# Kernel tuning notes

Measured on AMD Instinct MI355X. Metric: run time of the kernel, lower is better.

The kernel has to match this reference:

```python
import jax, jax.numpy as jnp
import numpy as np

N_NODES = 1000
N_EDGES = 8000
BATCH = 64
IN_DIM = 64
HID = 128
N_CLASSES = 2


def setup_inputs() -> dict:
    key = jax.random.key(0)
    ks = jax.random.split(key, 8)
    x = jax.random.normal(ks[0], (BATCH * N_NODES, IN_DIM), jnp.float32)
    # per-graph random edges, offset so each graph's nodes are disjoint
    ei = jax.random.randint(ks[1], (2, BATCH * N_EDGES), 0, N_NODES)
    offs = jnp.repeat(jnp.arange(BATCH) * N_NODES, N_EDGES)
    edge_index = (ei + offs[None, :]).astype(jnp.int32)
    batch = jnp.repeat(jnp.arange(BATCH), N_NODES).astype(jnp.int32)
    # learnable params (init is ones in source; use uniform [0,1.3] to exercise
    # both the <0.2 zeroing branch and the clamp-at-1 branch)
    edge_weights = jax.random.uniform(ks[2], (N_EDGES,), jnp.float32, 0.0, 1.3)
    node_importance = jax.random.uniform(ks[3], (N_NODES,), jnp.float32, 0.0, 1.3)
    s1 = 1.0 / np.sqrt(IN_DIM)
    W1 = jax.random.uniform(ks[4], (IN_DIM, HID), jnp.float32, -s1, s1)
    b1 = jnp.zeros((HID,), jnp.float32)
    sn = 1.0 / np.sqrt(HID * N_NODES)
    Wn = jax.random.uniform(ks[5], (HID * N_NODES, 32), jnp.float32, -sn, sn)
    bn = jnp.zeros((32,), jnp.float32)
    sc = 1.0 / np.sqrt(32)
    Wc = jax.random.uniform(ks[6], (32, N_CLASSES), jnp.float32, -sc, sc)
    bc = jnp.zeros((N_CLASSES,), jnp.float32)
    return dict(x=x, edge_index=edge_index, batch=batch,
                edge_weights=edge_weights, node_importance=node_importance,
                W1=W1, b1=b1, Wn=Wn, bn=bn, Wc=Wc, bc=bc)


def _gcn(x, src, dst, ew, W, b, n):
    """PyG GCNConv: add self-loops (weight 1), symmetric normalization, linear."""
    loop = jnp.arange(n, dtype=src.dtype)
    src = jnp.concatenate([src, loop])
    dst = jnp.concatenate([dst, loop])
    ew = jnp.concatenate([ew, jnp.ones((n,), ew.dtype)])
    deg = jax.ops.segment_sum(ew, dst, num_segments=n)
    dinv = jnp.where(deg > 0, jax.lax.rsqrt(jnp.maximum(deg, 1e-12)), 0.0)
    norm = dinv[src] * ew * dinv[dst]          # [E+n]
    h = x @ W                                  # [n, HID]
    out = jax.ops.segment_sum(h[src] * norm[:, None], dst, num_segments=n)
    return out + b


def reference(x, edge_index, batch, edge_weights, node_importance,
              W1, b1, Wn, bn, Wc, bc):
    # edge sparsification: zero below 0.2, clamp above at 1
    ew = jnp.where(edge_weights < 0.2, 0.0, jnp.minimum(edge_weights, 1.0))
    ni_clamped = jnp.clip(node_importance, 0.0, 1.0)
    B = edge_index.shape[1] // N_EDGES
    n_total = x.shape[0]
    exp_ew = jnp.tile(ew, B)
    # source uses the RAW (unclamped) node_importance here - replicated
    exp_ni = jnp.tile(node_importance, B)[:, None]
    h = x * exp_ni
    h = _gcn(h, edge_index[0], edge_index[1], exp_ew, W1, b1, n_total)
    h = jax.nn.relu(h)
    # each graph has exactly N_NODES nodes and batch is sorted, so the
    # per-graph mask+pad loop is exactly a reshape
    g = h.reshape(B, N_NODES * h.shape[1])     # [B, N*HID]
    g = g @ Wn + bn                            # [B, 32]
    out = g @ Wc + bc                          # [B, N_CLASSES]
    return (out, ew, ni_clamped)
```

## Files before the change

### kernel.cpp

```cpp
#include <hip/hip_runtime.h>

#define N_NODES_C 1000
#define N_EDGES_C 8000
#define BATCH_C   64
#define IN_DIM_C  64
#define HID_C     128
#define NT (BATCH_C * N_NODES_C)
#define ET (BATCH_C * N_EDGES_C)

#define WS_DEG    0
#define WS_EWS    64000
#define WS_ROWP   72000
#define WS_PEDGE  137536
#define WS_PART   1161536
#define WS_H2     1685824

__global__ __launch_bounds__(256) void prep(const float* __restrict__ ew_in,
                                            const float* __restrict__ ni,
                                            float* __restrict__ ws,
                                            float* __restrict__ out) {
    int i = blockIdx.x * 256 + threadIdx.x;
    if (i < N_EDGES_C) {
        float w = ew_in[i];
        float s = (w < 0.2f) ? 0.0f : fminf(w, 1.0f);
        ws[WS_EWS + i] = s;
        out[128 + i] = s;
    }
    if (i < N_NODES_C) {
        float v = ni[i];
        out[128 + N_EDGES_C + i] = fminf(fmaxf(v, 0.0f), 1.0f);
    }
}

__global__ __launch_bounds__(256) void deg_csr(const int* __restrict__ ei,
                                               float* __restrict__ ws) {
    __shared__ float dacc[N_NODES_C];
    __shared__ int   cnt[N_NODES_C];
    __shared__ int   rs[N_NODES_C + 8];
    __shared__ int   wtot[4];
    int g = blockIdx.x, tid = threadIdx.x;
    int lane = tid & 63, wid = tid >> 6;
    int ebase = g * N_EDGES_C, gbase = g * N_NODES_C;
    const float* ews = ws + WS_EWS;

    for (int i = tid; i < N_NODES_C; i += 256) { dacc[i] = 1.0f; cnt[i] = 0; }
    __syncthreads();

    for (int le = tid; le < N_EDGES_C; le += 256) {
        int dl = ei[ET + ebase + le] - gbase;
        atomicAdd(&dacc[dl], ews[le]);
        atomicAdd(&cnt[dl], 1);
    }
    __syncthreads();

    for (int i = tid; i < N_NODES_C; i += 256) {
        float d = rsqrtf(dacc[i]);
        dacc[i] = d;
        ws[WS_DEG + gbase + i] = d;
    }

    int s0 = 0, s1 = 0, s2 = 0, s3 = 0, tsum = 0;
    if (tid < 250) {
        s0 = cnt[4 * tid]; s1 = cnt[4 * tid + 1];
        s2 = cnt[4 * tid + 2]; s3 = cnt[4 * tid + 3];
        tsum = s0 + s1 + s2 + s3;
    }
    int v = tsum;
    #pragma unroll
    for (int off = 1; off < 64; off <<= 1) {
        int n = __shfl_up(v, off, 64);
        if (lane >= off) v += n;
    }
    if (lane == 63) wtot[wid] = v;
    __syncthreads();
    int base = 0;
    for (int w = 0; w < wid; ++w) base += wtot[w];
    int excl = base + v - tsum;
    if (tid < 250) {
        rs[4 * tid]     = excl;
        rs[4 * tid + 1] = excl + s0;
        rs[4 * tid + 2] = excl + s0 + s1;
        rs[4 * tid + 3] = excl + s0 + s1 + s2;
    }
    if (tid == 255) rs[N_NODES_C] = N_EDGES_C;
    __syncthreads();

    int* rowp = (int*)(ws + WS_ROWP);
    for (int i = tid; i <= N_NODES_C; i += 256) rowp[g * 1024 + i] = rs[i];
    for (int i = tid; i < N_NODES_C; i += 256) cnt[i] = rs[i];
    __syncthreads();

    int2* pedge = (int2*)(ws + WS_PEDGE);
    for (int le = tid; le < N_EDGES_C; le += 256) {
        int s  = ei[ebase + le];
        int dl = ei[ET + ebase + le] - gbase;
        float nm = dacc[s - gbase] * ews[le] * dacc[dl];
        int pos = atomicAdd(&cnt[dl], 1);
        pedge[ebase + pos] = make_int2(s, __float_as_int(nm));
    }
}

__global__ __launch_bounds__(256) void gemm_h2(const float* __restrict__ x,
                                               const float* __restrict__ ni,
                                               const float* __restrict__ W1,
                                               float* __restrict__ h2) {
    __shared__ float xs[128][65];
    __shared__ float wsm[64 * 128];
    int tid = threadIdx.x;
    int base = blockIdx.x * 128;

    #pragma unroll
    for (int i = 0; i < 8; ++i) {
        int idx = i * 1024 + tid * 4;
        int r = idx >> 6, d = idx & 63;
        float4 v = *(const float4*)&x[(base + r) * 64 + d];
        float s = ni[(base + r) % N_NODES_C];
        xs[r][d + 0] = v.x * s;
        xs[r][d + 1] = v.y * s;
        xs[r][d + 2] = v.z * s;
        xs[r][d + 3] = v.w * s;
    }
    #pragma unroll
    for (int i = 0; i < 8; ++i) {
        int idx = i * 1024 + tid * 4;
        *(float4*)&wsm[idx] = *(const float4*)&W1[idx];
    }
    __syncthreads();

    int tx = tid & 15, ty = tid >> 4;
    int r0 = ty * 8, c0 = tx * 8;
    float acc[8][8];
    #pragma unroll
    for (int i = 0; i < 8; ++i)
        #pragma unroll
        for (int j = 0; j < 8; ++j) acc[i][j] = 0.0f;

    for (int d = 0; d < 64; ++d) {
        float a[8];
        #pragma unroll
        for (int i = 0; i < 8; ++i) a[i] = xs[r0 + i][d];
        float4 b0 = *(float4*)&wsm[d * 128 + c0];
        float4 b1 = *(float4*)&wsm[d * 128 + c0 + 4];
        float b[8] = {b0.x, b0.y, b0.z, b0.w, b1.x, b1.y, b1.z, b1.w};
        #pragma unroll
        for (int i = 0; i < 8; ++i)
            #pragma unroll
            for (int j = 0; j < 8; ++j)
                acc[i][j] = fmaf(a[i], b[j], acc[i][j]);
    }

    #pragma unroll
    for (int i = 0; i < 8; ++i) {
        float* dst = &h2[(base + r0 + i) * HID_C + c0];
        float4 o0 = {acc[i][0], acc[i][1], acc[i][2], acc[i][3]};
        float4 o1 = {acc[i][4], acc[i][5], acc[i][6], acc[i][7]};
        *(float4*)dst = o0;
        *(float4*)(dst + 4) = o1;
    }
}

__global__ __launch_bounds__(256) void spmm(const float* __restrict__ ws_ro,
                                            float* __restrict__ h2,
                                            const float* __restrict__ b1) {
    __shared__ float res[N_NODES_C * 16];
    int bid = blockIdx.x;
    int g  = bid & 63;
    int c0 = (bid >> 6) * 16;
    int tid = threadIdx.x;
    int fq = tid & 3, dslot = tid >> 2;

    const int*  rowp  = (const int*)(ws_ro + WS_ROWP) + g * 1024;
    const int2* pedge = (const int2*)(ws_ro + WS_PEDGE) + g * N_EDGES_C;
    const float* dinv = ws_ro + WS_DEG;
    int gbase = g * N_NODES_C;

    for (int iter = 0; iter < 16; ++iter) {
        int d = iter * 64 + dslot;
        if (d < N_NODES_C) {
            int e0 = rowp[d], e1 = rowp[d + 1];
            float4 a = make_float4(0.f, 0.f, 0.f, 0.f);
            for (int e = e0; e < e1; ++e) {
                int2 ed = pedge[e];
                float nm = __int_as_float(ed.y);
                float4 hv = *(const float4*)&h2[ed.x * HID_C + c0 + fq * 4];
                a.x = fmaf(hv.x, nm, a.x);
                a.y = fmaf(hv.y, nm, a.y);
                a.z = fmaf(hv.z, nm, a.z);
                a.w = fmaf(hv.w, nm, a.w);
            }
            *(float4*)&res[d * 16 + fq * 4] = a;
        }
    }
    __syncthreads();

    for (int idx = tid; idx < N_NODES_C * 16; idx += 256) {
        int v = idx >> 4, f = idx & 15;
        int node = gbase + v;
        float dv = dinv[node];
        float val = res[idx] + h2[node * HID_C + c0 + f] * (dv * dv) + b1[c0 + f];
        h2[node * HID_C + c0 + f] = fmaxf(val, 0.0f);
    }
}

__global__ __launch_bounds__(256) void reduce_g(const float* __restrict__ rh,
                                                const float* __restrict__ Wn,
                                                float* __restrict__ part) {
    int tid = threadIdx.x;
    int j = tid & 31, bg = tid >> 5;
    int k0 = blockIdx.x * 500;
    float acc[8] = {0, 0, 0, 0, 0, 0, 0, 0};
    for (int kk = 0; kk < 500; kk += 4) {
        int k = k0 + kk;
        float w0 = Wn[(k + 0) * 32 + j];
        float w1 = Wn[(k + 1) * 32 + j];
        float w2 = Wn[(k + 2) * 32 + j];
        float w3 = Wn[(k + 3) * 32 + j];
        #pragma unroll
        for (int u = 0; u < 8; ++u) {
            float4 r = *(const float4*)&rh[(bg * 8 + u) * 128000 + k];
            acc[u] = fmaf(r.x, w0, acc[u]);
            acc[u] = fmaf(r.y, w1, acc[u]);
            acc[u] = fmaf(r.z, w2, acc[u]);
            acc[u] = fmaf(r.w, w3, acc[u]);
        }
    }
    #pragma unroll
    for (int u = 0; u < 8; ++u)
        part[blockIdx.x * 2048 + (bg * 8 + u) * 32 + j] = acc[u];
}

__global__ __launch_bounds__(256) void final_out(const float* __restrict__ ws_ro,
                                                 const float* __restrict__ bn,
                                                 const float* __restrict__ Wc,
                                                 const float* __restrict__ bc,
                                                 float* __restrict__ out) {
    int gid = blockIdx.x * 256 + threadIdx.x;
    int g = gid >> 5, j = gid & 31;
    const float* part = ws_ro + WS_PART;
    float s = 0.0f;
    for (int c = 0; c < 256; ++c)
        s += part[c * 2048 + gid];
    float gv = s + bn[j];
    float o0 = gv * Wc[j * 2 + 0];
    float o1 = gv * Wc[j * 2 + 1];
    #pragma unroll
    for (int off = 16; off >= 1; off >>= 1) {
        o0 += __shfl_xor(o0, off);
        o1 += __shfl_xor(o1, off);
    }
    if (j == 0) {
        out[g * 2 + 0] = o0 + bc[0];
        out[g * 2 + 1] = o1 + bc[1];
    }
}

extern "C" void kernel_launch(void* const* d_in, const int* in_sizes, int n_in,
                              void* d_out, int out_size, void* d_ws, size_t ws_size,
                              hipStream_t stream) {
    const float* x  = (const float*)d_in[0];
    const int*   ei = (const int*)d_in[1];
    const float* ew = (const float*)d_in[3];
    const float* ni = (const float*)d_in[4];
    const float* W1 = (const float*)d_in[5];
    const float* b1 = (const float*)d_in[6];
    const float* Wn = (const float*)d_in[7];
    const float* bn = (const float*)d_in[8];
    const float* Wc = (const float*)d_in[9];
    const float* bc = (const float*)d_in[10];
    float* out = (float*)d_out;
    float* ws  = (float*)d_ws;

    prep<<<32, 256, 0, stream>>>(ew, ni, ws, out);
    gemm_h2<<<NT / 128, 256, 0, stream>>>(x, ni, W1, ws + WS_H2);
    deg_csr<<<BATCH_C, 256, 0, stream>>>(ei, ws);
    spmm<<<BATCH_C * 8, 256, 0, stream>>>(ws, ws + WS_H2, b1);
    reduce_g<<<256, 256, 0, stream>>>(ws + WS_H2, Wn, ws + WS_PART);
    final_out<<<8, 256, 0, stream>>>(ws, bn, Wc, bc, out);
}
```

Before: 293.3 us.

## Split CSR build into grid-wide kernels and add out-of-place SpMM path

Replaces the per-graph single-block degree/CSR kernel (64 blocks) with three grid-wide kernels: a global-atomic degree/count pass, a per-graph scan, and a global-atomic scatter. When the workspace is large enough, a new out-of-place SpMM runs with one thread per (node, 16-feature chunk) and writes to a separate buffer, so it needs no shared staging and no block-wide sync. Otherwise an in-place fallback runs with 1024-thread blocks. The aim is better GPU occupancy for the graph preprocessing and aggregation, at the cost of extra launches and contended global atomics.

Measured after the change: 258.9 us. 1.13x faster.

```diff
diff --git a/kernel.cpp b/kernel.cpp
--- a/kernel.cpp
+++ b/kernel.cpp
@@ -10,16 +10,23 @@
 
 #define WS_DEG    0
 #define WS_EWS    64000
-#define WS_ROWP   72000
-#define WS_PEDGE  137536
-#define WS_PART   1161536
-#define WS_H2     1685824
+#define WS_CNT    72000
+#define WS_CUR    136000
+#define WS_ROWP   200000
+#define WS_PEDGE  265536
+#define WS_PART   1289536
+#define WS_H2     1813824
+#define WS_RH     10005824
 
 __global__ __launch_bounds__(256) void prep(const float* __restrict__ ew_in,
                                             const float* __restrict__ ni,
                                             float* __restrict__ ws,
                                             float* __restrict__ out) {
     int i = blockIdx.x * 256 + threadIdx.x;
+    if (i < NT) {
+        ws[WS_DEG + i] = 1.0f;
+        ((int*)(ws + WS_CNT))[i] = 0;
+    }
     if (i < N_EDGES_C) {
         float w = ew_in[i];
         float s = (w < 0.2f) ? 0.0f : fminf(w, 1.0f);
@@ -32,32 +39,25 @@
     }
 }
 
-__global__ __launch_bounds__(256) void deg_csr(const int* __restrict__ ei,
+__global__ __launch_bounds__(256) void deg_cnt(const int* __restrict__ ei,
                                                float* __restrict__ ws) {
-    __shared__ float dacc[N_NODES_C];
-    __shared__ int   cnt[N_NODES_C];
-    __shared__ int   rs[N_NODES_C + 8];
-    __shared__ int   wtot[4];
+    int e = blockIdx.x * 256 + threadIdx.x;
+    int d = ei[ET + e];
+    int le = e % N_EDGES_C;
+    atomicAdd(&ws[WS_DEG + d], ws[WS_EWS + le]);
+    atomicAdd(&((int*)(ws + WS_CNT))[d], 1);
+}
+
+__global__ __launch_bounds__(256) void csr_scan(float* __restrict__ ws) {
+    __shared__ int rs[N_NODES_C + 8];
+    __shared__ int wtot[4];
     int g = blockIdx.x, tid = threadIdx.x;
     int lane = tid & 63, wid = tid >> 6;
-    int ebase = g * N_EDGES_C, gbase = g * N_NODES_C;
-    const float* ews = ws + WS_EWS;
-
-    for (int i = tid; i < N_NODES_C; i += 256) { dacc[i] = 1.0f; cnt[i] = 0; }
-    __syncthreads();
-
-    for (int le = tid; le < N_EDGES_C; le += 256) {
-        int dl = ei[ET + ebase + le] - gbase;
-        atomicAdd(&dacc[dl], ews[le]);
-        atomicAdd(&cnt[dl], 1);
-    }
-    __syncthreads();
-
-    for (int i = tid; i < N_NODES_C; i += 256) {
-        float d = rsqrtf(dacc[i]);
-        dacc[i] = d;
-        ws[WS_DEG + gbase + i] = d;
-    }
+    int gbase = g * N_NODES_C;
+    const int* cnt = (const int*)(ws + WS_CNT) + gbase;
+
+    for (int i = tid; i < N_NODES_C; i += 256)
+        ws[WS_DEG + gbase + i] = rsqrtf(ws[WS_DEG + gbase + i]);
 
     int s0 = 0, s1 = 0, s2 = 0, s3 = 0, tsum = 0;
     if (tid < 250) {
@@ -85,19 +85,24 @@
     if (tid == 255) rs[N_NODES_C] = N_EDGES_C;
     __syncthreads();
 
-    int* rowp = (int*)(ws + WS_ROWP);
-    for (int i = tid; i <= N_NODES_C; i += 256) rowp[g * 1024 + i] = rs[i];
-    for (int i = tid; i < N_NODES_C; i += 256) cnt[i] = rs[i];
-    __syncthreads();
-
-    int2* pedge = (int2*)(ws + WS_PEDGE);
-    for (int le = tid; le < N_EDGES_C; le += 256) {
-        int s  = ei[ebase + le];
-        int dl = ei[ET + ebase + le] - gbase;
-        float nm = dacc[s - gbase] * ews[le] * dacc[dl];
-        int pos = atomicAdd(&cnt[dl], 1);
-        pedge[ebase + pos] = make_int2(s, __float_as_int(nm));
-    }
+    int* rowp = (int*)(ws + WS_ROWP) + g * 1024;
+    int* cur  = (int*)(ws + WS_CUR) + gbase;
+    for (int i = tid; i <= N_NODES_C; i += 256) rowp[i] = rs[i];
+    for (int i = tid; i < N_NODES_C; i += 256) cur[i] = rs[i];
+}
+
+__global__ __launch_bounds__(256) void scatter(const int* __restrict__ ei,
+                                               float* __restrict__ ws) {
+    int e = blockIdx.x * 256 + threadIdx.x;
+    int g = e / N_EDGES_C;
+    int le = e - g * N_EDGES_C;
+    int s = ei[e];
+    int d = ei[ET + e];
+    const float* dinv = ws + WS_DEG;
+    float nm = dinv[s] * ws[WS_EWS + le] * dinv[d];
+    int pos = atomicAdd(&((int*)(ws + WS_CUR))[d], 1);
+    ((int2*)(ws + WS_PEDGE))[g * N_EDGES_C + pos] =
+        make_int2(s, __float_as_int(nm));
 }
 
 __global__ __launch_bounds__(256) void gemm_h2(const float* __restrict__ x,
@@ -159,9 +164,62 @@
     }
 }
 
-__global__ __launch_bounds__(256) void spmm(const float* __restrict__ ws_ro,
-                                            float* __restrict__ h2,
-                                            const float* __restrict__ b1) {
+__global__ __launch_bounds__(256) void spmm_op(const float* __restrict__ ws_ro,
+                                               const float* __restrict__ h2,
+                                               const float* __restrict__ b1,
+                                               float* __restrict__ rh) {
+    int bid = blockIdx.x;
+    int g = bid & 63, slice = bid >> 6;
+    int t = threadIdx.x;
+    if (t >= 250) return;
+    int p = slice * 250 + t;
+    int dst = p >> 3, chunk = p & 7, c0 = chunk << 4;
+
+    const int*  rowp  = (const int*)(ws_ro + WS_ROWP) + g * 1024;
+    const int2* pedge = (const int2*)(ws_ro + WS_PEDGE) + g * N_EDGES_C;
+    const float* dinv = ws_ro + WS_DEG;
+
+    int e0 = rowp[dst], e1 = rowp[dst + 1];
+    float4 a0 = {0,0,0,0}, a1 = {0,0,0,0}, a2 = {0,0,0,0}, a3 = {0,0,0,0};
+    for (int e = e0; e < e1; ++e) {
+        int2 ed = pedge[e];
+        float nm = __int_as_float(ed.y);
+        const float* hp = &h2[ed.x * HID_C + c0];
+        float4 h0 = *(const float4*)(hp + 0);
+        float4 h1 = *(const float4*)(hp + 4);
+        float4 h2v = *(const float4*)(hp + 8);
+        float4 h3 = *(const float4*)(hp + 12);
+        a0.x = fmaf(h0.x, nm, a0.x); a0.y = fmaf(h0.y, nm, a0.y);
+        a0.z = fmaf(h0.z, nm, a0.z); a0.w = fmaf(h0.w, nm, a0.w);
+        a1.x = fmaf(h1.x, nm, a1.x); a1.y = fmaf(h1.y, nm, a1.y);
+        a1.z = fmaf(h1.z, nm, a1.z); a1.w = fmaf(h1.w, nm, a1.w);
+        a2.x = fmaf(h2v.x, nm, a2.x); a2.y = fmaf(h2v.y, nm, a2.y);
+        a2.z = fmaf(h2v.z, nm, a2.z); a2.w = fmaf(h2v.w, nm, a2.w);
+        a3.x = fmaf(h3.x, nm, a3.x); a3.y = fmaf(h3.y, nm, a3.y);
+        a3.z = fmaf(h3.z, nm, a3.z); a3.w = fmaf(h3.w, nm, a3.w);
+    }
+
+    int node = g * N_NODES_C + dst;
+    float dv = dinv[node], dv2 = dv * dv;
+    const float* sp = &h2[node * HID_C + c0];
+    float* op = &rh[node * HID_C + c0];
+    #pragma unroll
+    for (int q = 0; q < 4; ++q) {
+        float4 sv = *(const float4*)(sp + q * 4);
+        float4 bv = *(const float4*)&b1[c0 + q * 4];
+        float4 av = q == 0 ? a0 : q == 1 ? a1 : q == 2 ? a2 : a3;
+        float4 o;
+        o.x = fmaxf(fmaf(sv.x, dv2, av.x) + bv.x, 0.0f);
+        o.y = fmaxf(fmaf(sv.y, dv2, av.y) + bv.y, 0.0f);
+        o.z = fmaxf(fmaf(sv.z, dv2, av.z) + bv.z, 0.0f);
+        o.w = fmaxf(fmaf(sv.w, dv2, av.w) + bv.w, 0.0f);
+        *(float4*)(op + q * 4) = o;
+    }
+}
+
+__global__ __launch_bounds__(1024) void spmm_ip(const float* __restrict__ ws_ro,
+                                                float* __restrict__ h2,
+                                                const float* __restrict__ b1) {
     __shared__ float res[N_NODES_C * 16];
     int bid = blockIdx.x;
     int g  = bid & 63;
@@ -174,8 +232,8 @@
     const float* dinv = ws_ro + WS_DEG;
     int gbase = g * N_NODES_C;
 
-    for (int iter = 0; iter < 16; ++iter) {
-        int d = iter * 64 + dslot;
+    for (int iter = 0; iter < 4; ++iter) {
+        int d = iter * 256 + dslot;
         if (d < N_NODES_C) {
             int e0 = rowp[d], e1 = rowp[d + 1];
             float4 a = make_float4(0.f, 0.f, 0.f, 0.f);
@@ -193,7 +251,7 @@
     }
     __syncthreads();
 
-    for (int idx = tid; idx < N_NODES_C * 16; idx += 256) {
+    for (int idx = tid; idx < N_NODES_C * 16; idx += 1024) {
         int v = idx >> 4, f = idx & 15;
         int node = gbase + v;
         float dv = dinv[node];
@@ -270,10 +328,19 @@
     float* out = (float*)d_out;
     float* ws  = (float*)d_ws;
 
-    prep<<<32, 256, 0, stream>>>(ew, ni, ws, out);
-    gemm_h2<<<NT / 128, 256, 0, stream>>>(x, ni, W1, ws + WS_H2);
-    deg_csr<<<BATCH_C, 256, 0, stream>>>(ei, ws);
-    spmm<<<BATCH_C * 8, 256, 0, stream>>>(ws, ws + WS_H2, b1);
-    reduce_g<<<256, 256, 0, stream>>>(ws + WS_H2, Wn, ws + WS_PART);
+    bool big = ws_size >= (size_t)(WS_RH + 8192000) * sizeof(float);
+    float* h2 = ws + WS_H2;
+    float* rh = big ? ws + WS_RH : h2;
+
+    prep<<<NT / 256, 256, 0, stream>>>(ew, ni, ws, out);
+    gemm_h2<<<NT / 128, 256, 0, stream>>>(x, ni, W1, h2);
+    deg_cnt<<<ET / 256, 256, 0, stream>>>(ei, ws);
+    csr_scan<<<BATCH_C, 256, 0, stream>>>(ws);
+    scatter<<<ET / 256, 256, 0, stream>>>(ei, ws);
+    if (big)
+        spmm_op<<<BATCH_C * 32, 256, 0, stream>>>(ws, h2, b1, rh);
+    else
+        spmm_ip<<<BATCH_C * 8, 1024, 0, stream>>>(ws, h2, b1);
+    reduce_g<<<256, 256, 0, stream>>>(rh, Wn, ws + WS_PART);
     final_out<<<8, 256, 0, stream>>>(ws, bn, Wc, bc, out);
 }
```
